# Optimization experiments

Measured on AMD Instinct MI355X. Metric: run time of the kernel, lower is better.

## Reference

```python
import jax, jax.numpy as jnp
import numpy as np

# static config matching init_kwargs / input_specs
D = 768      # dim
H = 12       # num_heads
HD = D // H  # head_dim = 64
C = 38       # in_chans (AlternatingAttention default)
B = 4
T = 256
N = C * T    # 9728
SCALE = HD ** -0.5
EPS = 1e-5   # LayerNorm eps
HID = 4 * D  # mlp hidden


def setup_inputs() -> dict:
    key = jax.random.key(0)
    ks = jax.random.split(key, 6)
    w = lambda k, sh: (jax.random.normal(k, sh, jnp.float32) * 0.02)
    return {
        "x": jax.random.normal(ks[0], (B, N, D), jnp.float32),
        "norm1_w": jnp.ones((D,), jnp.float32),
        "norm1_b": jnp.zeros((D,), jnp.float32),
        "qkv_w": w(ks[1], (3 * D, D)),            # nn.Linear(dim, 3*dim, bias=False)
        "proj_w": w(ks[2], (D, D)),
        "proj_b": jnp.zeros((D,), jnp.float32),
        "norm2_w": jnp.ones((D,), jnp.float32),
        "norm2_b": jnp.zeros((D,), jnp.float32),
        "fc1_w": w(ks[3], (HID, D)),
        "fc1_b": jnp.zeros((HID,), jnp.float32),
        "fc2_w": w(ks[4], (D, HID)),
        "fc2_b": jnp.zeros((D,), jnp.float32),
    }


def _ln(x, w, b):
    m = x.mean(-1, keepdims=True)
    v = ((x - m) ** 2).mean(-1, keepdims=True)
    return (x - m) * jax.lax.rsqrt(v + EPS) * w + b


def _attn(x, qkv_w, proj_w, proj_b):
    # x: (Bc, Nn, D) -- manual (non-fused) SDPA as in the torch module
    Bc, Nn, _ = x.shape
    qkv = (x @ qkv_w.T).reshape(Bc, Nn, 3, H, HD)
    q, k, v = jnp.moveaxis(qkv, 2, 0)             # each (Bc, Nn, H, HD)
    q = jnp.swapaxes(q, 1, 2) * SCALE             # (Bc, H, Nn, HD)
    k = jnp.swapaxes(k, 1, 2)
    v = jnp.swapaxes(v, 1, 2)
    attn = jax.nn.softmax(q @ jnp.swapaxes(k, -2, -1), axis=-1)  # (Bc,H,Nn,Nn)
    o = attn @ v                                  # (Bc, H, Nn, HD)
    o = jnp.swapaxes(o, 1, 2).reshape(Bc, Nn, D)
    return o @ proj_w.T + proj_b


def reference(x, norm1_w, norm1_b, qkv_w, proj_w, proj_b,
              norm2_w, norm2_b, fc1_w, fc1_b, fc2_w, fc2_b):
    # Attention branch: block_idx=1 -> time-axis attention
    h = _ln(x, norm1_w, norm1_b)
    h = h.reshape(B, C, T, D).reshape(B * C, T, D)   # 'B (C T) D -> (B C) T D'
    h = _attn(h, qkv_w, proj_w, proj_b)
    h = h.reshape(B, C, T, D).reshape(B, N, D)       # '(B C) T D -> B (C T) D'
    x = x + h                                        # ls1 = Identity, drop_path = Identity
    # MLP branch
    h2 = _ln(x, norm2_w, norm2_b)
    h2 = jax.nn.gelu(h2 @ fc1_w.T + fc1_b, approximate=False)
    h2 = h2 @ fc2_w.T + fc2_b
    return x + h2
```

## Files before the change

### kernel.cpp

```cpp
#include <hip/hip_runtime.h>
#include <stdint.h>

#define DD 768
#define HH 12
#define HDIM 64
#define TT 256
#define BCN 152
#define MROWS 38912
#define HID 3072

typedef __attribute__((ext_vector_type(8))) short bf16x8;
typedef __attribute__((ext_vector_type(4))) float f32x4;

__device__ __forceinline__ float b2f(unsigned short u) {
  union { unsigned int i; float f; } c; c.i = ((unsigned int)u) << 16; return c.f;
}
__device__ __forceinline__ unsigned short f2b(float f) {
  union { float f; unsigned int i; } c; c.f = f;
  unsigned int x = c.i;
  return (unsigned short)((x + 0x7fffu + ((x >> 16) & 1u)) >> 16);
}

__device__ __forceinline__ void gload16(const unsigned short* g, unsigned short* l) {
  __builtin_amdgcn_global_load_lds(
      (const __attribute__((address_space(1))) void*)g,
      (__attribute__((address_space(3))) void*)l, 16, 0, 0);
}

__global__ __launch_bounds__(256) void k_cvt(const float* __restrict__ in,
                                             unsigned short* __restrict__ out, int n4) {
  int i = blockIdx.x * 256 + threadIdx.x;
  if (i >= n4) return;
  float4 a = ((const float4*)in)[i];
  ushort4 u;
  u.x = f2b(a.x); u.y = f2b(a.y); u.z = f2b(a.z); u.w = f2b(a.w);
  ((ushort4*)out)[i] = u;
}

__global__ __launch_bounds__(256) void k_ln(const float* __restrict__ x,
                                            const float* __restrict__ w,
                                            const float* __restrict__ b,
                                            unsigned short* __restrict__ out) {
  int lane = threadIdx.x & 63;
  int wv = threadIdx.x >> 6;
  size_t row = (size_t)blockIdx.x * 4 + wv;
  const float4* xr = (const float4*)(x + row * DD);
  float4 v0 = xr[lane], v1 = xr[lane + 64], v2 = xr[lane + 128];
  float s = v0.x + v0.y + v0.z + v0.w + v1.x + v1.y + v1.z + v1.w + v2.x + v2.y + v2.z + v2.w;
  float q = v0.x*v0.x + v0.y*v0.y + v0.z*v0.z + v0.w*v0.w
          + v1.x*v1.x + v1.y*v1.y + v1.z*v1.z + v1.w*v1.w
          + v2.x*v2.x + v2.y*v2.y + v2.z*v2.z + v2.w*v2.w;
#pragma unroll
  for (int m = 1; m < 64; m <<= 1) { s += __shfl_xor(s, m, 64); q += __shfl_xor(q, m, 64); }
  float mean = s * (1.0f / 768.0f);
  float var = q * (1.0f / 768.0f) - mean * mean;
  float rstd = rsqrtf(var + 1e-5f);
  ushort4* orow = (ushort4*)(out + row * DD);
#pragma unroll
  for (int i = 0; i < 3; i++) {
    int idx = lane + i * 64;
    float4 v = (i == 0) ? v0 : (i == 1) ? v1 : v2;
    float4 ww = ((const float4*)w)[idx];
    float4 bb = ((const float4*)b)[idx];
    ushort4 u;
    u.x = f2b((v.x - mean) * rstd * ww.x + bb.x);
    u.y = f2b((v.y - mean) * rstd * ww.y + bb.y);
    u.z = f2b((v.z - mean) * rstd * ww.z + bb.z);
    u.w = f2b((v.w - mean) * rstd * ww.w + bb.w);
    orow[idx] = u;
  }
}

template <int MODE>
__global__ __launch_bounds__(256, 4) void k_gemm6(const unsigned short* __restrict__ A,
                                                  const unsigned short* __restrict__ W,
                                                  const float* __restrict__ bias,
                                                  const float* resid,
                                                  void* outv, int N, int K) {
  __shared__ __align__(16) unsigned short As[128 * 64];
  __shared__ __align__(16) unsigned short Bs[128 * 64];
  const int tid = threadIdx.x;
  const int lane = tid & 63, wv = tid >> 6;
  const int wr = wv >> 1, wc = wv & 1;
  const int cl = lane & 15, hi = lane >> 4;

  const int nbx = gridDim.x;
  const int nwg = nbx * gridDim.y;
  const int flat = blockIdx.y * nbx + blockIdx.x;
  const int swz = (flat & 7) * (nwg >> 3) + (flat >> 3);
  const size_t bm = (size_t)(swz / nbx) * 128;
  const size_t bn = (size_t)(swz % nbx) * 128;
  const unsigned short* Ab = A + bm * K;
  const unsigned short* Wb = W + bn * K;

  f32x4 acc[4][4];
#pragma unroll
  for (int m = 0; m < 4; m++)
#pragma unroll
    for (int n = 0; n < 4; n++) acc[m][n] = (f32x4){0.f, 0.f, 0.f, 0.f};

  const int nk = K >> 6;
  for (int kt = 0; kt < nk; ++kt) {
    __syncthreads();
#pragma unroll
    for (int i = 0; i < 4; i++) {
      int g = i * 256 + tid;
      int row = g >> 3;
      int cg = (g & 7) ^ (row & 7);
      gload16(Ab + (size_t)row * K + (size_t)kt * 64 + cg * 8, &As[g * 8]);
      gload16(Wb + (size_t)row * K + (size_t)kt * 64 + cg * 8, &Bs[g * 8]);
    }
    __syncthreads();
#pragma unroll
    for (int ks = 0; ks < 2; ++ks) {
      bf16x8 af[4], bfr[4];
#pragma unroll
      for (int m = 0; m < 4; m++) {
        int row = wr * 64 + m * 16 + cl;
        af[m] = *(const bf16x8*)&As[row * 64 + (((ks * 4 + hi) ^ (row & 7)) * 8)];
      }
#pragma unroll
      for (int n = 0; n < 4; n++) {
        int row = wc * 64 + n * 16 + cl;
        bfr[n] = *(const bf16x8*)&Bs[row * 64 + (((ks * 4 + hi) ^ (row & 7)) * 8)];
      }
#pragma unroll
      for (int m = 0; m < 4; m++)
#pragma unroll
        for (int n = 0; n < 4; n++)
          acc[m][n] = __builtin_amdgcn_mfma_f32_16x16x32_bf16(af[m], bfr[n], acc[m][n], 0, 0, 0);
    }
  }

#pragma unroll
  for (int m = 0; m < 4; m++) {
#pragma unroll
    for (int n = 0; n < 4; n++) {
      size_t col = bn + wc * 64 + n * 16 + cl;
#pragma unroll
      for (int r = 0; r < 4; r++) {
        size_t row = bm + wr * 64 + m * 16 + hi * 4 + r;
        float v = acc[m][n][r];
        if (MODE == 0) {
          ((unsigned short*)outv)[row * N + col] = f2b(v);
        } else if (MODE == 1) {
          v += bias[col] + resid[row * N + col];
          ((float*)outv)[row * N + col] = v;
        } else {
          v += bias[col];
          float g = 0.5f * v * (1.0f + erff(v * 0.70710678118654752f));
          ((unsigned short*)outv)[row * N + col] = f2b(g);
        }
      }
    }
  }
}

__global__ __launch_bounds__(256) void k_attn(const unsigned short* __restrict__ qkv,
                                              unsigned short* __restrict__ o) {
  __shared__ unsigned short Kc[64 * 64];
  __shared__ unsigned short Vt[64 * 64];
  __shared__ unsigned short Pl[4][64 * 64];
  int h = blockIdx.x;
  int bc = blockIdx.y;
  int tid = threadIdx.x;
  int lane = tid & 63, wv = tid >> 6;
  int cl = lane & 15, hi = lane >> 4;

  bf16x8 qf[4][2];
#pragma unroll
  for (int m = 0; m < 4; m++)
#pragma unroll
    for (int ks = 0; ks < 2; ks++) {
      size_t row = (size_t)bc * 256 + wv * 64 + m * 16 + cl;
      bf16x8 raw = *(const bf16x8*)(qkv + row * 2304 + h * 64 + ks * 32 + hi * 8);
      bf16x8 sc;
#pragma unroll
      for (int j = 0; j < 8; j++) sc[j] = (short)f2b(0.125f * b2f((unsigned short)raw[j]));
      qf[m][ks] = sc;
    }

  f32x4 oacc[4][4];
#pragma unroll
  for (int m = 0; m < 4; m++)
#pragma unroll
    for (int n = 0; n < 4; n++) oacc[m][n] = (f32x4){0.f, 0.f, 0.f, 0.f};
  float mrun[4][4], lrun[4][4];
#pragma unroll
  for (int m = 0; m < 4; m++)
#pragma unroll
    for (int r = 0; r < 4; r++) { mrun[m][r] = -1e30f; lrun[m][r] = 0.f; }

  for (int j = 0; j < 4; j++) {
    __syncthreads();
#pragma unroll
    for (int it = 0; it < 2; ++it) {
      int idx = it * 256 + tid;
      int tok = idx >> 3;
      int c8 = idx & 7;
      size_t gtok = (size_t)bc * 256 + j * 64 + tok;
      uint4 kvv = *(const uint4*)(qkv + gtok * 2304 + 768 + h * 64 + c8 * 8);
      *(uint4*)&Kc[tok * 64 + c8 * 8] = kvv;
      union { uint4 u4; unsigned short us[8]; } cv;
      cv.u4 = *(const uint4*)(qkv + gtok * 2304 + 1536 + h * 64 + c8 * 8);
#pragma unroll
      for (int jj = 0; jj < 8; jj++) Vt[(c8 * 8 + jj) * 64 + tok] = cv.us[jj];
    }
    __syncthreads();

    f32x4 s[4][4];
#pragma unroll
    for (int m = 0; m < 4; m++)
#pragma unroll
      for (int n = 0; n < 4; n++) s[m][n] = (f32x4){0.f, 0.f, 0.f, 0.f};
#pragma unroll
    for (int ks = 0; ks < 2; ++ks) {
      int ko = ks * 32 + hi * 8;
      bf16x8 kf[4];
#pragma unroll
      for (int n = 0; n < 4; n++) kf[n] = *(const bf16x8*)&Kc[(n * 16 + cl) * 64 + ko];
#pragma unroll
      for (int m = 0; m < 4; m++)
#pragma unroll
        for (int n = 0; n < 4; n++)
          s[m][n] = __builtin_amdgcn_mfma_f32_16x16x32_bf16(qf[m][ks], kf[n], s[m][n], 0, 0, 0);
    }

#pragma unroll
    for (int m = 0; m < 4; m++) {
#pragma unroll
      for (int r = 0; r < 4; r++) {
        float pm = fmaxf(fmaxf(s[m][0][r], s[m][1][r]), fmaxf(s[m][2][r], s[m][3][r]));
#pragma unroll
        for (int xm = 1; xm < 16; xm <<= 1) pm = fmaxf(pm, __shfl_xor(pm, xm, 64));
        float nm = fmaxf(mrun[m][r], pm);
        float fac = __expf(mrun[m][r] - nm);
        mrun[m][r] = nm;
        float ps = 0.f;
#pragma unroll
        for (int n = 0; n < 4; n++) {
          float e = __expf(s[m][n][r] - nm);
          s[m][n][r] = e;
          ps += e;
        }
#pragma unroll
        for (int xm = 1; xm < 16; xm <<= 1) ps += __shfl_xor(ps, xm, 64);
        lrun[m][r] = lrun[m][r] * fac + ps;
#pragma unroll
        for (int n2 = 0; n2 < 4; n2++) oacc[m][n2][r] *= fac;
      }
#pragma unroll
      for (int n = 0; n < 4; n++)
#pragma unroll
        for (int r = 0; r < 4; r++)
          Pl[wv][(m * 16 + hi * 4 + r) * 64 + n * 16 + cl] = f2b(s[m][n][r]);
    }
    __syncthreads();

#pragma unroll
    for (int ks = 0; ks < 2; ++ks) {
      int ko = ks * 32 + hi * 8;
      bf16x8 pa[4], pv[4];
#pragma unroll
      for (int m = 0; m < 4; m++) pa[m] = *(const bf16x8*)&Pl[wv][(m * 16 + cl) * 64 + ko];
#pragma unroll
      for (int n = 0; n < 4; n++) pv[n] = *(const bf16x8*)&Vt[(n * 16 + cl) * 64 + ko];
#pragma unroll
      for (int m = 0; m < 4; m++)
#pragma unroll
        for (int n = 0; n < 4; n++)
          oacc[m][n] = __builtin_amdgcn_mfma_f32_16x16x32_bf16(pa[m], pv[n], oacc[m][n], 0, 0, 0);
    }
  }

#pragma unroll
  for (int m = 0; m < 4; m++)
#pragma unroll
    for (int r = 0; r < 4; r++) {
      float inv = 1.0f / lrun[m][r];
      size_t row = (size_t)bc * 256 + wv * 64 + m * 16 + hi * 4 + r;
#pragma unroll
      for (int n = 0; n < 4; n++)
        o[row * DD + h * 64 + n * 16 + cl] = f2b(oacc[m][n][r] * inv);
    }
}

extern "C" void kernel_launch(void* const* d_in, const int* in_sizes, int n_in,
                              void* d_out, int out_size, void* d_ws, size_t ws_size,
                              hipStream_t stream) {
  const float* x     = (const float*)d_in[0];
  const float* n1w   = (const float*)d_in[1];
  const float* n1b   = (const float*)d_in[2];
  const float* qkvw  = (const float*)d_in[3];
  const float* projw = (const float*)d_in[4];
  const float* projb = (const float*)d_in[5];
  const float* n2w   = (const float*)d_in[6];
  const float* n2b   = (const float*)d_in[7];
  const float* fc1w  = (const float*)d_in[8];
  const float* fc1b  = (const float*)d_in[9];
  const float* fc2w  = (const float*)d_in[10];
  const float* fc2b  = (const float*)d_in[11];
  float* out = (float*)d_out;

  const size_t NEED = 312999936ull;
  if (ws_size < NEED) return;
  char* ws = (char*)d_ws;
  unsigned short* h   = (unsigned short*)(ws);
  unsigned short* qkv = (unsigned short*)(ws + 59768832ull);
  unsigned short* ob  = (unsigned short*)(ws + 239075328ull);
  unsigned short* act = (unsigned short*)(ws + 59768832ull);
  unsigned short* wq  = (unsigned short*)(ws + 298844160ull);
  unsigned short* wp  = wq + 2304 * 768;
  unsigned short* w1  = wp + 768 * 768;
  unsigned short* w2  = w1 + 3072 * 768;

  k_cvt<<<1728, 256, 0, stream>>>(qkvw, wq, 2304 * 768 / 4);
  k_cvt<<<576, 256, 0, stream>>>(projw, wp, 768 * 768 / 4);
  k_cvt<<<2304, 256, 0, stream>>>(fc1w, w1, 3072 * 768 / 4);
  k_cvt<<<2304, 256, 0, stream>>>(fc2w, w2, 768 * 3072 / 4);

  k_ln<<<MROWS / 4, 256, 0, stream>>>(x, n1w, n1b, h);
  k_gemm6<0><<<dim3(2304 / 128, MROWS / 128), 256, 0, stream>>>(h, wq, nullptr, nullptr, qkv, 2304, 768);
  k_attn<<<dim3(HH, BCN), 256, 0, stream>>>(qkv, ob);
  k_gemm6<1><<<dim3(768 / 128, MROWS / 128), 256, 0, stream>>>(ob, wp, projb, x, out, 768, 768);
  k_ln<<<MROWS / 4, 256, 0, stream>>>(out, n2w, n2b, h);
  k_gemm6<2><<<dim3(3072 / 128, MROWS / 128), 256, 0, stream>>>(h, w1, fc1b, nullptr, act, 3072, 768);
  k_gemm6<1><<<dim3(768 / 128, MROWS / 128), 256, 0, stream>>>(act, w2, fc2b, out, out, 768, 3072);
}
```

Baseline: 1.137 ms.

## Restructure attention kernel: 8 waves, double-buffered K, swizzled LDS, prefetched V

Rewrites the flash-attention kernel to use 512 threads, with each wave owning 32 query rows instead of 64. K tiles are double-buffered through async global-to-LDS loads, and V is prefetched into registers one tile ahead. K, V-transpose and P buffers use XOR swizzles to avoid LDS bank conflicts. The P buffer is cut to a per-wave 16x64 slab and reused per m-subtile, which adds a wait and a schedule barrier. The aim is to overlap global loads with compute and raise occupancy, at the cost of more sync points and tricky index math. The attention kernel is only part of the total pipeline.

```diff
diff --git a/kernel.cpp b/kernel.cpp
--- a/kernel.cpp
+++ b/kernel.cpp
@@ -156,78 +156,93 @@
   }
 }
 
-__global__ __launch_bounds__(256) void k_attn(const unsigned short* __restrict__ qkv,
+__global__ __launch_bounds__(512) void k_attn(const unsigned short* __restrict__ qkv,
                                               unsigned short* __restrict__ o) {
-  __shared__ unsigned short Kc[64 * 64];
-  __shared__ unsigned short Vt[64 * 64];
-  __shared__ unsigned short Pl[4][64 * 64];
-  int h = blockIdx.x;
-  int bc = blockIdx.y;
-  int tid = threadIdx.x;
-  int lane = tid & 63, wv = tid >> 6;
-  int cl = lane & 15, hi = lane >> 4;
-
-  bf16x8 qf[4][2];
-#pragma unroll
-  for (int m = 0; m < 4; m++)
+  __shared__ __align__(16) unsigned short Kc[2][64 * 64];
+  __shared__ __align__(16) unsigned short Vt[64 * 64];
+  __shared__ __align__(16) unsigned short Pl[8][16 * 64];
+  const int h = blockIdx.x, bc = blockIdx.y;
+  const int tid = threadIdx.x;
+  const int lane = tid & 63, wv = tid >> 6;
+  const int cl = lane & 15, hi = lane >> 4;
+
+  bf16x8 qf[2][2];
+#pragma unroll
+  for (int m = 0; m < 2; m++)
 #pragma unroll
     for (int ks = 0; ks < 2; ks++) {
-      size_t row = (size_t)bc * 256 + wv * 64 + m * 16 + cl;
+      size_t row = (size_t)bc * 256 + wv * 32 + m * 16 + cl;
       bf16x8 raw = *(const bf16x8*)(qkv + row * 2304 + h * 64 + ks * 32 + hi * 8);
       bf16x8 sc;
 #pragma unroll
-      for (int j = 0; j < 8; j++) sc[j] = (short)f2b(0.125f * b2f((unsigned short)raw[j]));
+      for (int jx = 0; jx < 8; jx++) sc[jx] = (short)f2b(0.125f * b2f((unsigned short)raw[jx]));
       qf[m][ks] = sc;
     }
 
-  f32x4 oacc[4][4];
-#pragma unroll
-  for (int m = 0; m < 4; m++)
+  f32x4 oacc[2][4];
+#pragma unroll
+  for (int m = 0; m < 2; m++)
 #pragma unroll
     for (int n = 0; n < 4; n++) oacc[m][n] = (f32x4){0.f, 0.f, 0.f, 0.f};
-  float mrun[4][4], lrun[4][4];
-#pragma unroll
-  for (int m = 0; m < 4; m++)
+  float mrun[2][4], lrun[2][4];
+#pragma unroll
+  for (int m = 0; m < 2; m++)
 #pragma unroll
     for (int r = 0; r < 4; r++) { mrun[m][r] = -1e30f; lrun[m][r] = 0.f; }
+
+  auto stageK = [&](int j, int buf) {
+    int tok = tid >> 3, c8 = tid & 7;
+    size_t gtok = (size_t)bc * 256 + j * 64 + tok;
+    gload16(qkv + gtok * 2304 + 768 + h * 64 + ((c8 ^ (tok & 7)) * 8), &Kc[buf][tid * 8]);
+  };
+  uint4 vreg[2];
+  auto loadV = [&](int j, int slot) {
+    int tok = tid >> 3, c8 = tid & 7;
+    size_t gtok = (size_t)bc * 256 + j * 64 + tok;
+    vreg[slot] = *(const uint4*)(qkv + gtok * 2304 + 1536 + h * 64 + c8 * 8);
+  };
+  auto writeV = [&](int slot) {
+    int tok = tid >> 3, c8 = tid & 7;
+    union { uint4 u4; unsigned short us[8]; } cv; cv.u4 = vreg[slot];
+#pragma unroll
+    for (int jj = 0; jj < 8; jj++) {
+      int d = c8 * 8 + jj;
+      int g = ((tok >> 3) ^ (d & 7) ^ ((d >> 3) & 7)) & 7;
+      Vt[d * 64 + g * 8 + (tok & 7)] = cv.us[jj];
+    }
+  };
+
+  stageK(0, 0);
+  loadV(0, 0);
 
   for (int j = 0; j < 4; j++) {
     __syncthreads();
-#pragma unroll
-    for (int it = 0; it < 2; ++it) {
-      int idx = it * 256 + tid;
-      int tok = idx >> 3;
-      int c8 = idx & 7;
-      size_t gtok = (size_t)bc * 256 + j * 64 + tok;
-      uint4 kvv = *(const uint4*)(qkv + gtok * 2304 + 768 + h * 64 + c8 * 8);
-      *(uint4*)&Kc[tok * 64 + c8 * 8] = kvv;
-      union { uint4 u4; unsigned short us[8]; } cv;
-      cv.u4 = *(const uint4*)(qkv + gtok * 2304 + 1536 + h * 64 + c8 * 8);
-#pragma unroll
-      for (int jj = 0; jj < 8; jj++) Vt[(c8 * 8 + jj) * 64 + tok] = cv.us[jj];
-    }
-    __syncthreads();
-
-    f32x4 s[4][4];
-#pragma unroll
-    for (int m = 0; m < 4; m++)
+
+    f32x4 s[2][4];
+#pragma unroll
+    for (int m = 0; m < 2; m++)
 #pragma unroll
       for (int n = 0; n < 4; n++) s[m][n] = (f32x4){0.f, 0.f, 0.f, 0.f};
 #pragma unroll
     for (int ks = 0; ks < 2; ++ks) {
-      int ko = ks * 32 + hi * 8;
       bf16x8 kf[4];
 #pragma unroll
-      for (int n = 0; n < 4; n++) kf[n] = *(const bf16x8*)&Kc[(n * 16 + cl) * 64 + ko];
-#pragma unroll
-      for (int m = 0; m < 4; m++)
+      for (int n = 0; n < 4; n++) {
+        int row = n * 16 + cl;
+        kf[n] = *(const bf16x8*)&Kc[j & 1][row * 64 + (((ks * 4 + hi) ^ (row & 7)) * 8)];
+      }
+#pragma unroll
+      for (int m = 0; m < 2; m++)
 #pragma unroll
         for (int n = 0; n < 4; n++)
           s[m][n] = __builtin_amdgcn_mfma_f32_16x16x32_bf16(qf[m][ks], kf[n], s[m][n], 0, 0, 0);
     }
 
-#pragma unroll
-    for (int m = 0; m < 4; m++) {
+    stageK((j + 1) & 3, (j + 1) & 1);
+    loadV((j + 1) & 3, (j + 1) & 1);
+
+#pragma unroll
+    for (int m = 0; m < 2; m++) {
 #pragma unroll
       for (int r = 0; r < 4; r++) {
         float pm = fmaxf(fmaxf(s[m][0][r], s[m][1][r]), fmaxf(s[m][2][r], s[m][3][r]));
@@ -249,36 +264,48 @@
 #pragma unroll
         for (int n2 = 0; n2 < 4; n2++) oacc[m][n2][r] *= fac;
       }
+    }
+
+    writeV(j & 1);
+    __syncthreads();
+
+    bf16x8 pv[2][4];
+#pragma unroll
+    for (int ks = 0; ks < 2; ks++)
+#pragma unroll
+      for (int n = 0; n < 4; n++) {
+        int d = n * 16 + cl;
+        pv[ks][n] = *(const bf16x8*)&Vt[d * 64 + ((((ks * 4 + hi) ^ (d & 7) ^ ((d >> 3) & 7)) & 7) * 8)];
+      }
+#pragma unroll
+    for (int m = 0; m < 2; m++) {
 #pragma unroll
       for (int n = 0; n < 4; n++)
 #pragma unroll
-        for (int r = 0; r < 4; r++)
-          Pl[wv][(m * 16 + hi * 4 + r) * 64 + n * 16 + cl] = f2b(s[m][n][r]);
-    }
-    __syncthreads();
-
-#pragma unroll
-    for (int ks = 0; ks < 2; ++ks) {
-      int ko = ks * 32 + hi * 8;
-      bf16x8 pa[4], pv[4];
-#pragma unroll
-      for (int m = 0; m < 4; m++) pa[m] = *(const bf16x8*)&Pl[wv][(m * 16 + cl) * 64 + ko];
-#pragma unroll
-      for (int n = 0; n < 4; n++) pv[n] = *(const bf16x8*)&Vt[(n * 16 + cl) * 64 + ko];
-#pragma unroll
-      for (int m = 0; m < 4; m++)
-#pragma unroll
-        for (int n = 0; n < 4; n++)
-          oacc[m][n] = __builtin_amdgcn_mfma_f32_16x16x32_bf16(pa[m], pv[n], oacc[m][n], 0, 0, 0);
+        for (int r = 0; r < 4; r++) {
+          int q = hi * 4 + r;
+          int g = ((n * 2 + (cl >> 3)) ^ (q & 7) ^ (q >> 3)) & 7;
+          Pl[wv][q * 64 + g * 8 + (cl & 7)] = f2b(s[m][n][r]);
+        }
+      asm volatile("s_waitcnt lgkmcnt(0)" ::: "memory");
+      __builtin_amdgcn_sched_barrier(0);
+      bf16x8 pa0 = *(const bf16x8*)&Pl[wv][cl * 64 + (((hi ^ (cl & 7) ^ (cl >> 3)) & 7) * 8)];
+      bf16x8 pa1 = *(const bf16x8*)&Pl[wv][cl * 64 + ((((4 + hi) ^ (cl & 7) ^ (cl >> 3)) & 7) * 8)];
+#pragma unroll
+      for (int n = 0; n < 4; n++)
+        oacc[m][n] = __builtin_amdgcn_mfma_f32_16x16x32_bf16(pa0, pv[0][n], oacc[m][n], 0, 0, 0);
+#pragma unroll
+      for (int n = 0; n < 4; n++)
+        oacc[m][n] = __builtin_amdgcn_mfma_f32_16x16x32_bf16(pa1, pv[1][n], oacc[m][n], 0, 0, 0);
     }
   }
 
 #pragma unroll
-  for (int m = 0; m < 4; m++)
+  for (int m = 0; m < 2; m++)
 #pragma unroll
     for (int r = 0; r < 4; r++) {
       float inv = 1.0f / lrun[m][r];
-      size_t row = (size_t)bc * 256 + wv * 64 + m * 16 + hi * 4 + r;
+      size_t row = (size_t)bc * 256 + wv * 32 + m * 16 + hi * 4 + r;
 #pragma unroll
       for (int n = 0; n < 4; n++)
         o[row * DD + h * 64 + n * 16 + cl] = f2b(oacc[m][n][r] * inv);
@@ -321,7 +348,7 @@
 
   k_ln<<<MROWS / 4, 256, 0, stream>>>(x, n1w, n1b, h);
   k_gemm6<0><<<dim3(2304 / 128, MROWS / 128), 256, 0, stream>>>(h, wq, nullptr, nullptr, qkv, 2304, 768);
-  k_attn<<<dim3(HH, BCN), 256, 0, stream>>>(qkv, ob);
+  k_attn<<<dim3(HH, BCN), 512, 0, stream>>>(qkv, ob);
   k_gemm6<1><<<dim3(768 / 128, MROWS / 128), 256, 0, stream>>>(ob, wp, projb, x, out, 768, 768);
   k_ln<<<MROWS / 4, 256, 0, stream>>>(out, n2w, n2b, h);
   k_gemm6<2><<<dim3(3072 / 128, MROWS / 128), 256, 0, stream>>>(h, w1, fc1b, nullptr, act, 3072, 768);
```

New measurement: 1.012 ms. 1.12x faster.
